# Kernel tuning notes

Measured on AMD Instinct MI355X. Metric: run time of the kernel, lower is better.

## Reference

```python
import jax, jax.numpy as jnp
import numpy as np

K = 3  # knn interpolation neighbors (init kwarg k)
EPS = 1e-8


def _knn_interpolate(x, pos, pos_skip, B, k):
    # Uniform per-batch counts (guaranteed by setup_inputs) let us vectorize the
    # per-batch cdist+topk+gather chain as batched dense ops.
    Nc = pos.shape[0] // B
    Nf = pos_skip.shape[0] // B
    C = x.shape[1]
    pc = pos.reshape(B, Nc, 3)        # coarse positions
    pf = pos_skip.reshape(B, Nf, 3)   # fine (target) positions
    xc = x.reshape(B, Nc, C)          # coarse features
    # squared pairwise distances via gemm: [B, Nf, Nc]
    d2 = (jnp.sum(pf * pf, -1)[:, :, None]
          + jnp.sum(pc * pc, -1)[:, None, :]
          - 2.0 * jnp.einsum('bfd,bcd->bfc', pf, pc))
    _, idx = jax.lax.top_k(-d2, k)    # k nearest coarse indices per fine point
    b = jnp.arange(B)[:, None, None]
    nb_pos = pc[b, idx]                              # [B,Nf,k,3]
    diff = nb_pos - pf[:, :, None, :]
    dist = jnp.sqrt(jnp.sum(diff * diff, -1))        # exact same dist math as torch
    w = 1.0 / (dist + EPS)                           # [B,Nf,k]
    feats = xc[b, idx]                               # [B,Nf,k,C]
    num = jnp.einsum('bfkc,bfk->bfc', feats, w)
    den = jnp.sum(w, -1, keepdims=True) + EPS
    return (num / den).reshape(B * Nf, C)


def setup_inputs() -> dict:
    key = jax.random.key(0)
    ks = jax.random.split(key, 6)
    B, Nc, Nf, C, Cs, H = 16, 1024, 4096, 512, 256, 512
    x = jax.random.normal(ks[0], (B * Nc, C), jnp.float32)
    pos = jax.random.normal(ks[1], (B * Nc, 3), jnp.float32)
    batch = jnp.repeat(jnp.arange(B, dtype=jnp.int64), Nc)
    x_skip = jax.random.normal(ks[2], (B * Nf, Cs), jnp.float32)
    pos_skip = jax.random.normal(ks[3], (B * Nf, 3), jnp.float32)
    batch_skip = jnp.repeat(jnp.arange(B, dtype=jnp.int64), Nf)
    # MLP params (self.nn = MLP 768 -> 512 -> 512, ReLU)
    W1 = jax.random.normal(ks[4], (C + Cs, H), jnp.float32) / np.sqrt(C + Cs).astype(np.float32)
    b1 = jnp.zeros((H,), jnp.float32)
    W2 = jax.random.normal(ks[5], (H, H), jnp.float32) / np.sqrt(H).astype(np.float32)
    b2 = jnp.zeros((H,), jnp.float32)
    return dict(x=x, pos=pos, batch=batch, x_skip=x_skip, pos_skip=pos_skip,
                batch_skip=batch_skip, W1=W1, b1=b1, W2=W2, b2=b2)


def reference(x, pos, batch, x_skip, pos_skip, batch_skip, W1, b1, W2, b2):
    B = int(np.asarray(batch).max()) + 1
    h = _knn_interpolate(x, pos, pos_skip, B, K)   # [N_fine, C]
    h = jnp.concatenate([h, x_skip], axis=1)       # skip connection concat
    h = jax.nn.relu(h @ W1 + b1)
    h = jax.nn.relu(h @ W2 + b2)
    return h
```

## Files before the change

### kernel.cpp

```cpp
#include <hip/hip_runtime.h>
#include <stdint.h>

typedef __attribute__((ext_vector_type(8))) short short8;
typedef __attribute__((ext_vector_type(4))) float f32x4;

static __device__ __forceinline__ ushort f2bf(float f) {
  uint32_t u = __float_as_uint(f);
  uint32_t r = (u + 0x7FFFu + ((u >> 16) & 1u)) >> 16;
  return (ushort)r;
}
static __device__ __forceinline__ float bf2f(ushort h) {
  return __uint_as_float(((uint32_t)h) << 16);
}

static __device__ __forceinline__ void ins3b(double d, int i,
    double& b0, double& b1, double& b2, int& i0, int& i1, int& i2) {
  const bool c0 = d < b0, c1 = d < b1, c2 = d < b2;
  const double nb0 = c0 ? d : b0;
  const int    ni0 = c0 ? i : i0;
  const double nb1 = c0 ? b0 : (c1 ? d : b1);
  const int    ni1 = c0 ? i0 : (c1 ? i : i1);
  const double nb2 = c1 ? b1 : (c2 ? d : b2);
  const int    ni2 = c1 ? i1 : (c2 ? i : i2);
  b0 = nb0; b1 = nb1; b2 = nb2; i0 = ni0; i1 = ni1; i2 = ni2;
}

__global__ __launch_bounds__(256) void prep_kernel(
    const float* __restrict__ pos, const float* __restrict__ pos_skip,
    const float* __restrict__ x, const float* __restrict__ xs,
    const float* __restrict__ W1, const float* __restrict__ W2,
    int4* __restrict__ idx_out, float4* __restrict__ w_out,
    ushort* __restrict__ xbf, ushort* __restrict__ xsbf,
    ushort* __restrict__ W1at, ushort* __restrict__ W1bt,
    ushort* __restrict__ W2t)
{
  __shared__ float pc4[4096];
  if (blockIdx.x < 1024) {
    const int b   = blockIdx.x >> 6;
    const int blk = blockIdx.x & 63;
    for (int i = threadIdx.x; i < 1024; i += 256) {
      const float* ps = pos + (size_t)b * 3072 + i * 3;
      float4 v = { ps[0], ps[1], ps[2], 0.f };
      *(float4*)&pc4[i * 4] = v;
    }
    __syncthreads();

    const int p   = threadIdx.x >> 2;
    const int sub = threadIdx.x & 3;
    const int row = b * 4096 + blk * 64 + p;
    const float pxf = pos_skip[(size_t)row * 3 + 0];
    const float pyf = pos_skip[(size_t)row * 3 + 1];
    const float pzf = pos_skip[(size_t)row * 3 + 2];

    uint32_t c0 = 0xFFFFFFFFu, c1 = 0xFFFFFFFFu, c2 = 0xFFFFFFFFu, c3 = 0xFFFFFFFFu;
    auto ins4u = [&](uint32_t k) {
      const bool l0 = k < c0, l1 = k < c1, l2 = k < c2, l3 = k < c3;
      const uint32_t n0 = l0 ? k  : c0;
      const uint32_t n1 = l0 ? c0 : (l1 ? k : c1);
      const uint32_t n2 = l1 ? c1 : (l2 ? k : c2);
      const uint32_t n3 = l2 ? c2 : (l3 ? k : c3);
      c0 = n0; c1 = n1; c2 = n2; c3 = n3;
    };
#pragma unroll 4
    for (int j = 0; j < 256; ++j) {
      const int i = j * 4 + sub;
      const float4 q = *(const float4*)&pc4[i * 4];
      const float dx = q.x - pxf;
      const float dy = q.y - pyf;
      const float dz = q.z - pzf;
      const float d = fmaf(dx, dx, fmaf(dy, dy, dz * dz));
      ins4u((__float_as_uint(d) & 0xFFFFFC00u) | (uint32_t)i);
    }
#pragma unroll
    for (int m = 1; m <= 2; m <<= 1) {
      const uint32_t e0 = (uint32_t)__shfl_xor((int)c0, m);
      const uint32_t e1 = (uint32_t)__shfl_xor((int)c1, m);
      const uint32_t e2 = (uint32_t)__shfl_xor((int)c2, m);
      const uint32_t e3 = (uint32_t)__shfl_xor((int)c3, m);
      ins4u(e0); ins4u(e1); ins4u(e2); ins4u(e3);
    }
    if (sub == 0) {
      const double pxd = (double)pxf, pyd = (double)pyf, pzd = (double)pzf;
      auto exd = [&](int i) -> double {
        const double dx = (double)pc4[i * 4 + 0] - pxd;
        const double dy = (double)pc4[i * 4 + 1] - pyd;
        const double dz = (double)pc4[i * 4 + 2] - pzd;
        return dx * dx + dy * dy + dz * dz;
      };
      const int j0 = (int)(c0 & 1023u), j1 = (int)(c1 & 1023u);
      const int j2 = (int)(c2 & 1023u), j3 = (int)(c3 & 1023u);
      double b0 = 1e300, b1 = 1e300, b2 = 1e300;
      int i0 = 0, i1 = 0, i2 = 0;
      ins3b(exd(j0), j0, b0, b1, b2, i0, i1, i2);
      ins3b(exd(j1), j1, b0, b1, b2, i0, i1, i2);
      ins3b(exd(j2), j2, b0, b1, b2, i0, i1, i2);
      ins3b(exd(j3), j3, b0, b1, b2, i0, i1, i2);
      const double w0 = 1.0 / (sqrt(b0) + 1e-8);
      const double w1 = 1.0 / (sqrt(b1) + 1e-8);
      const double w2 = 1.0 / (sqrt(b2) + 1e-8);
      const double den = w0 + w1 + w2 + 1e-8;
      idx_out[row] = make_int4(i0, i1, i2, 0);
      w_out[row] = make_float4((float)(w0 / den), (float)(w1 / den), (float)(w2 / den), 0.f);
    }
  } else if (blockIdx.x < 3072) {
    const int id = (blockIdx.x - 1024) * 256 + threadIdx.x;
#pragma unroll
    for (int it = 0; it < 4; ++it) {
      const int i = id + it * 524288;
      const float4 v = *(const float4*)(x + (size_t)i * 4);
      ushort4 o = { f2bf(v.x), f2bf(v.y), f2bf(v.z), f2bf(v.w) };
      *(ushort4*)(xbf + (size_t)i * 4) = o;
    }
  } else if (blockIdx.x < 7168) {
    const int id = (blockIdx.x - 3072) * 256 + threadIdx.x;
#pragma unroll
    for (int it = 0; it < 4; ++it) {
      const int i = id + it * 1048576;
      const float4 v = *(const float4*)(xs + (size_t)i * 4);
      ushort4 o = { f2bf(v.x), f2bf(v.y), f2bf(v.z), f2bf(v.w) };
      *(ushort4*)(xsbf + (size_t)i * 4) = o;
    }
  } else {
    const int id = (blockIdx.x - 7168) * 256 + threadIdx.x;
    if (id < 262144) {
      const int n = id >> 9, k = id & 511;
      W1at[id] = f2bf(W1[(size_t)k * 512 + n]);
    } else if (id < 393216) {
      const int id2 = id - 262144;
      const int n = id2 >> 8, k = id2 & 255;
      W1bt[id2] = f2bf(W1[(size_t)(512 + k) * 512 + n]);
    } else if (id < 655360) {
      const int id3 = id - 393216;
      const int n = id3 >> 9, k = id3 & 511;
      W2t[id3] = f2bf(W2[(size_t)k * 512 + n]);
    }
  }
}

template<int K, bool OUT_BF16, bool ACT, bool COMBINE>
__global__ __launch_bounds__(512, 2) void gemm_bias_relu(
    const ushort* __restrict__ A, const ushort* __restrict__ Bt,
    const float* __restrict__ bias, void* __restrict__ Cout, int M, int N,
    const ushort* __restrict__ Ybf, const int4* __restrict__ idx3,
    const float4* __restrict__ w3)
{
  constexpr int BM = 256, BN = 256, BK = 64, NT = K / BK;
  __shared__ ushort Asm[2][BM * BK];
  __shared__ ushort Bsm[2][BN * BK];
  const int tid  = threadIdx.x;
  const int lane = tid & 63;
  const int wave = tid >> 6;

  const int cpx  = gridDim.x >> 3;
  const int wgid = (blockIdx.x & 7) * cpx + (blockIdx.x >> 3);
  const int nbn  = N / BN;
  const int bm   = wgid / nbn;
  const int bn   = wgid - bm * nbn;
  const int row0 = bm * BM, col0 = bn * BN;
  const int wr = wave >> 2, wc = wave & 3;
  const int sbase = wave * 4096 + lane * 16;

  f32x4 acc[8][4] = {};

  auto stageA = [&](int buf, int kt) {
#pragma unroll
    for (int i = 0; i < 4; ++i) {
      const int o = sbase + i * 1024;
      const int r = o >> 7, s = (o & 127) >> 4;
      __builtin_amdgcn_global_load_lds(
          (const __attribute__((address_space(1))) void*)(A + (size_t)(row0 + r) * K + kt * BK + ((s ^ (r & 7)) << 3)),
          (__attribute__((address_space(3))) void*)((char*)&Asm[buf][0] + o), 16, 0, 0);
    }
  };
  auto stageB = [&](int buf, int kt) {
#pragma unroll
    for (int i = 0; i < 4; ++i) {
      const int o = sbase + i * 1024;
      const int r = o >> 7, s = (o & 127) >> 4;
      __builtin_amdgcn_global_load_lds(
          (const __attribute__((address_space(1))) void*)(Bt + (size_t)(col0 + r) * K + kt * BK + ((s ^ (r & 7)) << 3)),
          (__attribute__((address_space(3))) void*)((char*)&Bsm[buf][0] + o), 16, 0, 0);
    }
  };
  auto rdA = [&](int buf, int mi, int kk) -> short8 {
    const int ra = wr * 128 + mi * 16 + (lane & 15);
    const int s  = kk * 4 + (lane >> 4);
    return *(const short8*)((const char*)&Asm[buf][0] + ra * 128 + ((s ^ (ra & 7)) << 4));
  };
  auto rdB = [&](int buf, int ni, int kk) -> short8 {
    const int rb = wc * 64 + ni * 16 + (lane & 15);
    const int s  = kk * 4 + (lane >> 4);
    return *(const short8*)((const char*)&Bsm[buf][0] + rb * 128 + ((s ^ (rb & 7)) << 4));
  };

  stageA(0, 0); stageB(0, 0);
  asm volatile("s_waitcnt vmcnt(0)" ::: "memory");
  __builtin_amdgcn_s_barrier();

  int cur = 0;
#pragma unroll 1
  for (int t = 0; t < NT; ++t) {
    short8 av[4], bv[4];
#pragma unroll
    for (int mi = 0; mi < 4; ++mi) av[mi] = rdA(cur, mi, 0);
#pragma unroll
    for (int ni = 0; ni < 4; ++ni) bv[ni] = rdB(cur, ni, 0);
    if (t + 1 < NT) stageA(cur ^ 1, t + 1);
    __builtin_amdgcn_s_barrier();
    asm volatile("s_waitcnt lgkmcnt(0)" ::: "memory");
    __builtin_amdgcn_sched_barrier(0);
    __builtin_amdgcn_s_setprio(1);
#pragma unroll
    for (int mi = 0; mi < 4; ++mi)
#pragma unroll
      for (int ni = 0; ni < 4; ++ni)
        acc[mi][ni] = __builtin_amdgcn_mfma_f32_16x16x32_bf16(av[mi], bv[ni], acc[mi][ni], 0, 0, 0);
    __builtin_amdgcn_s_setprio(0);
    __builtin_amdgcn_s_barrier();
#pragma unroll
    for (int mi = 0; mi < 4; ++mi) av[mi] = rdA(cur, 4 + mi, 0);
    if (t + 1 < NT) stageB(cur ^ 1, t + 1);
    __builtin_amdgcn_s_barrier();
    asm volatile("s_waitcnt lgkmcnt(0)" ::: "memory");
    __builtin_amdgcn_sched_barrier(0);
    __builtin_amdgcn_s_setprio(1);
#pragma unroll
    for (int mi = 0; mi < 4; ++mi)
#pragma unroll
      for (int ni = 0; ni < 4; ++ni)
        acc[4 + mi][ni] = __builtin_amdgcn_mfma_f32_16x16x32_bf16(av[mi], bv[ni], acc[4 + mi][ni], 0, 0, 0);
    __builtin_amdgcn_s_setprio(0);
    __builtin_amdgcn_s_barrier();
#pragma unroll
    for (int mi = 0; mi < 4; ++mi) av[mi] = rdA(cur, mi, 1);
#pragma unroll
    for (int ni = 0; ni < 4; ++ni) bv[ni] = rdB(cur, ni, 1);
    __builtin_amdgcn_s_barrier();
    asm volatile("s_waitcnt lgkmcnt(0)" ::: "memory");
    __builtin_amdgcn_sched_barrier(0);
    __builtin_amdgcn_s_setprio(1);
#pragma unroll
    for (int mi = 0; mi < 4; ++mi)
#pragma unroll
      for (int ni = 0; ni < 4; ++ni)
        acc[mi][ni] = __builtin_amdgcn_mfma_f32_16x16x32_bf16(av[mi], bv[ni], acc[mi][ni], 0, 0, 0);
    __builtin_amdgcn_s_setprio(0);
    __builtin_amdgcn_s_barrier();
#pragma unroll
    for (int mi = 0; mi < 4; ++mi) av[mi] = rdA(cur, 4 + mi, 1);
    __builtin_amdgcn_s_barrier();
    asm volatile("s_waitcnt lgkmcnt(0)" ::: "memory");
    __builtin_amdgcn_sched_barrier(0);
    __builtin_amdgcn_s_setprio(1);
#pragma unroll
    for (int mi = 0; mi < 4; ++mi)
#pragma unroll
      for (int ni = 0; ni < 4; ++ni)
        acc[4 + mi][ni] = __builtin_amdgcn_mfma_f32_16x16x32_bf16(av[mi], bv[ni], acc[4 + mi][ni], 0, 0, 0);
    __builtin_amdgcn_s_setprio(0);
    asm volatile("s_waitcnt vmcnt(0)" ::: "memory");
    __builtin_amdgcn_s_barrier();
    cur ^= 1;
  }

  const int lc = lane & 15, lr = lane >> 4;
  if constexpr (COMBINE) {
#pragma unroll
    for (int mi = 0; mi < 8; ++mi) {
#pragma unroll
      for (int r = 0; r < 4; ++r) {
        const int row = row0 + wr * 128 + mi * 16 + lr * 4 + r;
        const int4 id = idx3[row];
        const float4 w = w3[row];
        const ushort* Yb = Ybf + (size_t)(row >> 12) * 524288;
        const ushort* y0 = Yb + (size_t)id.x * 512;
        const ushort* y1 = Yb + (size_t)id.y * 512;
        const ushort* y2 = Yb + (size_t)id.z * 512;
#pragma unroll
        for (int ni = 0; ni < 4; ++ni) {
          const int col = col0 + wc * 64 + ni * 16 + lc;
          float v = acc[mi][ni][r]
                  + w.x * bf2f(y0[col])
                  + w.y * bf2f(y1[col])
                  + w.z * bf2f(y2[col])
                  + bias[col];
          v = v > 0.f ? v : 0.f;
          ((ushort*)Cout)[(size_t)row * 512 + col] = f2bf(v);
        }
      }
    }
  } else {
#pragma unroll
    for (int mi = 0; mi < 8; ++mi) {
#pragma unroll
      for (int ni = 0; ni < 4; ++ni) {
        const int col = col0 + wc * 64 + ni * 16 + lc;
        float bv2 = 0.f;
        if constexpr (ACT) bv2 = bias[col];
        const int rbase = row0 + wr * 128 + mi * 16 + lr * 4;
#pragma unroll
        for (int r = 0; r < 4; ++r) {
          float v = acc[mi][ni][r];
          if constexpr (ACT) { v += bv2; v = v > 0.f ? v : 0.f; }
          if (OUT_BF16) ((ushort*)Cout)[(size_t)(rbase + r) * N + col] = f2bf(v);
          else          ((float*)Cout)[(size_t)(rbase + r) * N + col] = v;
        }
      }
    }
  }
}

extern "C" void kernel_launch(void* const* d_in, const int* in_sizes, int n_in,
                              void* d_out, int out_size, void* d_ws, size_t ws_size,
                              hipStream_t stream) {
  const float* x        = (const float*)d_in[0];
  const float* pos      = (const float*)d_in[1];
  const float* x_skip   = (const float*)d_in[3];
  const float* pos_skip = (const float*)d_in[4];
  const float* W1       = (const float*)d_in[6];
  const float* b1       = (const float*)d_in[7];
  const float* W2       = (const float*)d_in[8];
  const float* b2       = (const float*)d_in[9];

  ushort* Ybf  = (ushort*)d_out;
  ushort* xbf  = (ushort*)((char*)d_out + 83886080);
  ushort* xsbf = (ushort*)((char*)d_out + 100663296);

  char* ws = (char*)d_ws;
  ushort* h2   = (ushort*)ws;
  ushort* W1at = (ushort*)(ws + 67108864);
  ushort* W1bt = (ushort*)(ws + 67633152);
  ushort* W2t  = (ushort*)(ws + 67895296);
  int4*   idx3 = (int4*)  (ws + 68419584);
  float4* w3   = (float4*)(ws + 69468160);

  prep_kernel<<<9728, 256, 0, stream>>>(pos, pos_skip, x, x_skip, W1, W2,
                                        idx3, w3, xbf, xsbf, W1at, W1bt, W2t);
  gemm_bias_relu<512, true, false, false><<<128, 512, 0, stream>>>(
      xbf, W1at, nullptr, (void*)Ybf, 16384, 512, nullptr, nullptr, nullptr);
  gemm_bias_relu<256, true, false, true><<<512, 512, 0, stream>>>(
      xsbf, W1bt, b1, (void*)h2, 65536, 512, Ybf, idx3, w3);
  gemm_bias_relu<512, false, true, false><<<512, 512, 0, stream>>>(
      h2, W2t, b2, d_out, 65536, 512, nullptr, nullptr, nullptr);
}
```

Baseline: 168.8 us.

## Fuse fp32-to-bf16 conversion of x and x_skip into GEMM A-tile staging

```diff
diff --git a/kernel.cpp b/kernel.cpp
--- a/kernel.cpp
+++ b/kernel.cpp
@@ -27,10 +27,8 @@
 
 __global__ __launch_bounds__(256) void prep_kernel(
     const float* __restrict__ pos, const float* __restrict__ pos_skip,
-    const float* __restrict__ x, const float* __restrict__ xs,
     const float* __restrict__ W1, const float* __restrict__ W2,
     int4* __restrict__ idx_out, float4* __restrict__ w_out,
-    ushort* __restrict__ xbf, ushort* __restrict__ xsbf,
     ushort* __restrict__ W1at, ushort* __restrict__ W1bt,
     ushort* __restrict__ W2t)
 {
@@ -102,26 +100,8 @@
       idx_out[row] = make_int4(i0, i1, i2, 0);
       w_out[row] = make_float4((float)(w0 / den), (float)(w1 / den), (float)(w2 / den), 0.f);
     }
-  } else if (blockIdx.x < 3072) {
+  } else {
     const int id = (blockIdx.x - 1024) * 256 + threadIdx.x;
-#pragma unroll
-    for (int it = 0; it < 4; ++it) {
-      const int i = id + it * 524288;
-      const float4 v = *(const float4*)(x + (size_t)i * 4);
-      ushort4 o = { f2bf(v.x), f2bf(v.y), f2bf(v.z), f2bf(v.w) };
-      *(ushort4*)(xbf + (size_t)i * 4) = o;
-    }
-  } else if (blockIdx.x < 7168) {
-    const int id = (blockIdx.x - 3072) * 256 + threadIdx.x;
-#pragma unroll
-    for (int it = 0; it < 4; ++it) {
-      const int i = id + it * 1048576;
-      const float4 v = *(const float4*)(xs + (size_t)i * 4);
-      ushort4 o = { f2bf(v.x), f2bf(v.y), f2bf(v.z), f2bf(v.w) };
-      *(ushort4*)(xsbf + (size_t)i * 4) = o;
-    }
-  } else {
-    const int id = (blockIdx.x - 7168) * 256 + threadIdx.x;
     if (id < 262144) {
       const int n = id >> 9, k = id & 511;
       W1at[id] = f2bf(W1[(size_t)k * 512 + n]);
@@ -137,9 +117,9 @@
   }
 }
 
-template<int K, bool OUT_BF16, bool ACT, bool COMBINE>
+template<int K, bool OUT_BF16, bool ACT, bool COMBINE, bool AF32>
 __global__ __launch_bounds__(512, 2) void gemm_bias_relu(
-    const ushort* __restrict__ A, const ushort* __restrict__ Bt,
+    const void* __restrict__ Av, const ushort* __restrict__ Bt,
     const float* __restrict__ bias, void* __restrict__ Cout, int M, int N,
     const ushort* __restrict__ Ybf, const int4* __restrict__ idx3,
     const float4* __restrict__ w3)
@@ -160,7 +140,12 @@
   const int wr = wave >> 2, wc = wave & 3;
   const int sbase = wave * 4096 + lane * 16;
 
+  const ushort* Abf = (const ushort*)Av;
+  const float*  Af  = (const float*)Av;
+  const int rl = tid >> 1, h = tid & 1;
+
   f32x4 acc[8][4] = {};
+  float4 ga[8];
 
   auto stageA = [&](int buf, int kt) {
 #pragma unroll
@@ -168,8 +153,27 @@
       const int o = sbase + i * 1024;
       const int r = o >> 7, s = (o & 127) >> 4;
       __builtin_amdgcn_global_load_lds(
-          (const __attribute__((address_space(1))) void*)(A + (size_t)(row0 + r) * K + kt * BK + ((s ^ (r & 7)) << 3)),
+          (const __attribute__((address_space(1))) void*)(Abf + (size_t)(row0 + r) * K + kt * BK + ((s ^ (r & 7)) << 3)),
           (__attribute__((address_space(3))) void*)((char*)&Asm[buf][0] + o), 16, 0, 0);
+    }
+  };
+  auto issueA = [&](int kt) {
+    const float* src = Af + (size_t)(row0 + rl) * K + kt * BK + h * 32;
+#pragma unroll
+    for (int q = 0; q < 8; ++q) ga[q] = *(const float4*)(src + q * 4);
+  };
+  auto writeA = [&](int buf) {
+    char* base = (char*)&Asm[buf][0] + rl * 128;
+#pragma unroll
+    for (int q2 = 0; q2 < 4; ++q2) {
+      const int s = h * 4 + q2;
+      short8 o;
+#pragma unroll
+      for (int e = 0; e < 4; ++e) {
+        o[e]     = (short)f2bf(((const float*)&ga[q2 * 2])[e]);
+        o[4 + e] = (short)f2bf(((const float*)&ga[q2 * 2 + 1])[e]);
+      }
+      *(short8*)(base + ((s ^ (rl & 7)) << 4)) = o;
     }
   };
   auto stageB = [&](int buf, int kt) {
@@ -193,8 +197,15 @@
     return *(const short8*)((const char*)&Bsm[buf][0] + rb * 128 + ((s ^ (rb & 7)) << 4));
   };
 
-  stageA(0, 0); stageB(0, 0);
-  asm volatile("s_waitcnt vmcnt(0)" ::: "memory");
+  if constexpr (AF32) {
+    issueA(0); stageB(0, 0);
+    asm volatile("s_waitcnt vmcnt(0)" ::: "memory");
+    writeA(0);
+    asm volatile("s_waitcnt lgkmcnt(0)" ::: "memory");
+  } else {
+    stageA(0, 0); stageB(0, 0);
+    asm volatile("s_waitcnt vmcnt(0)" ::: "memory");
+  }
   __builtin_amdgcn_s_barrier();
 
   int cur = 0;
@@ -205,7 +216,7 @@
     for (int mi = 0; mi < 4; ++mi) av[mi] = rdA(cur, mi, 0);
 #pragma unroll
     for (int ni = 0; ni < 4; ++ni) bv[ni] = rdB(cur, ni, 0);
-    if (t + 1 < NT) stageA(cur ^ 1, t + 1);
+    if (t + 1 < NT) { if constexpr (AF32) issueA(t + 1); else stageA(cur ^ 1, t + 1); }
     __builtin_amdgcn_s_barrier();
     asm volatile("s_waitcnt lgkmcnt(0)" ::: "memory");
     __builtin_amdgcn_sched_barrier(0);
@@ -258,7 +269,15 @@
       for (int ni = 0; ni < 4; ++ni)
         acc[4 + mi][ni] = __builtin_amdgcn_mfma_f32_16x16x32_bf16(av[mi], bv[ni], acc[4 + mi][ni], 0, 0, 0);
     __builtin_amdgcn_s_setprio(0);
-    asm volatile("s_waitcnt vmcnt(0)" ::: "memory");
+    if constexpr (AF32) {
+      if (t + 1 < NT) {
+        asm volatile("s_waitcnt vmcnt(0)" ::: "memory");
+        writeA(cur ^ 1);
+        asm volatile("s_waitcnt lgkmcnt(0)" ::: "memory");
+      }
+    } else {
+      asm volatile("s_waitcnt vmcnt(0)" ::: "memory");
+    }
     __builtin_amdgcn_s_barrier();
     cur ^= 1;
   }
@@ -323,8 +342,6 @@
   const float* b2       = (const float*)d_in[9];
 
   ushort* Ybf  = (ushort*)d_out;
-  ushort* xbf  = (ushort*)((char*)d_out + 83886080);
-  ushort* xsbf = (ushort*)((char*)d_out + 100663296);
 
   char* ws = (char*)d_ws;
   ushort* h2   = (ushort*)ws;
@@ -334,12 +351,12 @@
   int4*   idx3 = (int4*)  (ws + 68419584);
   float4* w3   = (float4*)(ws + 69468160);
 
-  prep_kernel<<<9728, 256, 0, stream>>>(pos, pos_skip, x, x_skip, W1, W2,
-                                        idx3, w3, xbf, xsbf, W1at, W1bt, W2t);
-  gemm_bias_relu<512, true, false, false><<<128, 512, 0, stream>>>(
-      xbf, W1at, nullptr, (void*)Ybf, 16384, 512, nullptr, nullptr, nullptr);
-  gemm_bias_relu<256, true, false, true><<<512, 512, 0, stream>>>(
-      xsbf, W1bt, b1, (void*)h2, 65536, 512, Ybf, idx3, w3);
-  gemm_bias_relu<512, false, true, false><<<512, 512, 0, stream>>>(
+  prep_kernel<<<3584, 256, 0, stream>>>(pos, pos_skip, W1, W2,
+                                        idx3, w3, W1at, W1bt, W2t);
+  gemm_bias_relu<512, true, false, false, true><<<128, 512, 0, stream>>>(
+      x, W1at, nullptr, (void*)Ybf, 16384, 512, nullptr, nullptr, nullptr);
+  gemm_bias_relu<256, true, false, true, true><<<512, 512, 0, stream>>>(
+      x_skip, W1bt, b1, (void*)h2, 65536, 512, Ybf, idx3, w3);
+  gemm_bias_relu<512, false, true, false, false><<<512, 512, 0, stream>>>(
       h2, W2t, b2, d_out, 65536, 512, nullptr, nullptr, nullptr);
 }
```

Measured after the change: 200.7 us. +18.9%, slower.

## Use dedicated 128x128-tile kernel for skip GEMM with fused KNN combine

Applied to the files above, without the earlier changes.

```diff
diff --git a/kernel.cpp b/kernel.cpp
--- a/kernel.cpp
+++ b/kernel.cpp
@@ -137,12 +137,10 @@
   }
 }
 
-template<int K, bool OUT_BF16, bool ACT, bool COMBINE>
+template<int K, bool OUT_BF16, bool ACT>
 __global__ __launch_bounds__(512, 2) void gemm_bias_relu(
     const ushort* __restrict__ A, const ushort* __restrict__ Bt,
-    const float* __restrict__ bias, void* __restrict__ Cout, int M, int N,
-    const ushort* __restrict__ Ybf, const int4* __restrict__ idx3,
-    const float4* __restrict__ w3)
+    const float* __restrict__ bias, void* __restrict__ Cout, int M, int N)
 {
   constexpr int BM = 256, BN = 256, BK = 64, NT = K / BK;
   __shared__ ushort Asm[2][BM * BK];
@@ -264,47 +262,121 @@
   }
 
   const int lc = lane & 15, lr = lane >> 4;
-  if constexpr (COMBINE) {
-#pragma unroll
-    for (int mi = 0; mi < 8; ++mi) {
+#pragma unroll
+  for (int mi = 0; mi < 8; ++mi) {
+#pragma unroll
+    for (int ni = 0; ni < 4; ++ni) {
+      const int col = col0 + wc * 64 + ni * 16 + lc;
+      float bv2 = 0.f;
+      if constexpr (ACT) bv2 = bias[col];
+      const int rbase = row0 + wr * 128 + mi * 16 + lr * 4;
 #pragma unroll
       for (int r = 0; r < 4; ++r) {
-        const int row = row0 + wr * 128 + mi * 16 + lr * 4 + r;
-        const int4 id = idx3[row];
-        const float4 w = w3[row];
-        const ushort* Yb = Ybf + (size_t)(row >> 12) * 524288;
-        const ushort* y0 = Yb + (size_t)id.x * 512;
-        const ushort* y1 = Yb + (size_t)id.y * 512;
-        const ushort* y2 = Yb + (size_t)id.z * 512;
-#pragma unroll
-        for (int ni = 0; ni < 4; ++ni) {
-          const int col = col0 + wc * 64 + ni * 16 + lc;
-          float v = acc[mi][ni][r]
-                  + w.x * bf2f(y0[col])
-                  + w.y * bf2f(y1[col])
-                  + w.z * bf2f(y2[col])
-                  + bias[col];
-          v = v > 0.f ? v : 0.f;
-          ((ushort*)Cout)[(size_t)row * 512 + col] = f2bf(v);
-        }
+        float v = acc[mi][ni][r];
+        if constexpr (ACT) { v += bv2; v = v > 0.f ? v : 0.f; }
+        if (OUT_BF16) ((ushort*)Cout)[(size_t)(rbase + r) * N + col] = f2bf(v);
+        else          ((float*)Cout)[(size_t)(rbase + r) * N + col] = v;
       }
     }
-  } else {
-#pragma unroll
-    for (int mi = 0; mi < 8; ++mi) {
+  }
+}
+
+__global__ __launch_bounds__(256, 2) void gemm128_combine(
+    const ushort* __restrict__ A, const ushort* __restrict__ Bt,
+    const float* __restrict__ bias, ushort* __restrict__ h2,
+    const ushort* __restrict__ Ybf, const int4* __restrict__ idx3,
+    const float4* __restrict__ w3)
+{
+  constexpr int K = 256, N = 512, BM = 128, BN = 128, BK = 64, NT = K / BK;
+  __shared__ ushort Asm[2][BM * BK];
+  __shared__ ushort Bsm[2][BN * BK];
+  const int tid  = threadIdx.x;
+  const int lane = tid & 63;
+  const int wave = tid >> 6;
+
+  const int cpx  = gridDim.x >> 3;
+  const int wgid = (blockIdx.x & 7) * cpx + (blockIdx.x >> 3);
+  const int nbn  = N / BN;
+  const int bm   = wgid / nbn;
+  const int bn   = wgid - bm * nbn;
+  const int row0 = bm * BM, col0 = bn * BN;
+  const int wr = wave >> 1, wc = wave & 1;
+  const int so = tid * 16;
+
+  f32x4 acc[4][4] = {};
+
+  auto stage = [&](int buf, int kt) {
+#pragma unroll
+    for (int i = 0; i < 4; ++i) {
+      const int o = i * 4096 + so;
+      const int r = o >> 7, s = (o & 127) >> 4;
+      const int cu = ((s ^ (r & 7)) << 3);
+      __builtin_amdgcn_global_load_lds(
+          (const __attribute__((address_space(1))) void*)(A + (size_t)(row0 + r) * K + kt * BK + cu),
+          (__attribute__((address_space(3))) void*)((char*)&Asm[buf][0] + o), 16, 0, 0);
+      __builtin_amdgcn_global_load_lds(
+          (const __attribute__((address_space(1))) void*)(Bt + (size_t)(col0 + r) * K + kt * BK + cu),
+          (__attribute__((address_space(3))) void*)((char*)&Bsm[buf][0] + o), 16, 0, 0);
+    }
+  };
+  auto compute = [&](int buf) {
+#pragma unroll
+    for (int kk = 0; kk < 2; ++kk) {
+      short8 af[4], bfr[4];
+#pragma unroll
+      for (int mi = 0; mi < 4; ++mi) {
+        const int ra = wr * 64 + mi * 16 + (lane & 15);
+        const int s  = kk * 4 + (lane >> 4);
+        af[mi] = *(const short8*)&Asm[buf][ra * BK + ((s ^ (ra & 7)) << 3)];
+      }
+#pragma unroll
+      for (int ni = 0; ni < 4; ++ni) {
+        const int rb = wc * 64 + ni * 16 + (lane & 15);
+        const int s  = kk * 4 + (lane >> 4);
+        bfr[ni] = *(const short8*)&Bsm[buf][rb * BK + ((s ^ (rb & 7)) << 3)];
+      }
+#pragma unroll
+      for (int mi = 0; mi < 4; ++mi)
+#pragma unroll
+        for (int ni = 0; ni < 4; ++ni)
+          acc[mi][ni] = __builtin_amdgcn_mfma_f32_16x16x32_bf16(af[mi], bfr[ni], acc[mi][ni], 0, 0, 0);
+    }
+  };
+
+  stage(0, 0);
+  __syncthreads();
+  int cur = 0;
+#pragma unroll 1
+  for (int kt = 0; kt < NT - 1; ++kt) {
+    stage(cur ^ 1, kt + 1);
+    compute(cur);
+    __syncthreads();
+    cur ^= 1;
+  }
+  compute(cur);
+
+  const int lc = lane & 15, lr = lane >> 4;
+#pragma unroll
+  for (int mi = 0; mi < 4; ++mi) {
+#pragma unroll
+    for (int r = 0; r < 4; ++r) {
+      const int row = row0 + wr * 64 + mi * 16 + lr * 4 + r;
+      const int4 id = idx3[row];
+      const float4 w = w3[row];
+      const ushort* Yb = Ybf + (size_t)(row >> 12) * 524288;
+      const ushort* y0 = Yb + (size_t)id.x * 512;
+      const ushort* y1 = Yb + (size_t)id.y * 512;
+      const ushort* y2 = Yb + (size_t)id.z * 512;
 #pragma unroll
       for (int ni = 0; ni < 4; ++ni) {
         const int col = col0 + wc * 64 + ni * 16 + lc;
-        float bv2 = 0.f;
-        if constexpr (ACT) bv2 = bias[col];
-        const int rbase = row0 + wr * 128 + mi * 16 + lr * 4;
-#pragma unroll
-        for (int r = 0; r < 4; ++r) {
-          float v = acc[mi][ni][r];
-          if constexpr (ACT) { v += bv2; v = v > 0.f ? v : 0.f; }
-          if (OUT_BF16) ((ushort*)Cout)[(size_t)(rbase + r) * N + col] = f2bf(v);
-          else          ((float*)Cout)[(size_t)(rbase + r) * N + col] = v;
-        }
+        float v = acc[mi][ni][r]
+                + w.x * bf2f(y0[col])
+                + w.y * bf2f(y1[col])
+                + w.z * bf2f(y2[col])
+                + bias[col];
+        v = v > 0.f ? v : 0.f;
+        h2[(size_t)row * 512 + col] = f2bf(v);
       }
     }
   }
@@ -336,10 +408,9 @@
 
   prep_kernel<<<9728, 256, 0, stream>>>(pos, pos_skip, x, x_skip, W1, W2,
                                         idx3, w3, xbf, xsbf, W1at, W1bt, W2t);
-  gemm_bias_relu<512, true, false, false><<<128, 512, 0, stream>>>(
-      xbf, W1at, nullptr, (void*)Ybf, 16384, 512, nullptr, nullptr, nullptr);
-  gemm_bias_relu<256, true, false, true><<<512, 512, 0, stream>>>(
-      xsbf, W1bt, b1, (void*)h2, 65536, 512, Ybf, idx3, w3);
-  gemm_bias_relu<512, false, true, false><<<512, 512, 0, stream>>>(
-      h2, W2t, b2, d_out, 65536, 512, nullptr, nullptr, nullptr);
-}
+  gemm_bias_relu<512, true, false><<<128, 512, 0, stream>>>(
+      xbf, W1at, nullptr, (void*)Ybf, 16384, 512);
+  gemm128_combine<<<2048, 256, 0, stream>>>(xsbf, W1bt, b1, h2, Ybf, idx3, w3);
+  gemm_bias_relu<512, false, true><<<512, 512, 0, stream>>>(
+      h2, W2t, b2, d_out, 65536, 512);
+}
```

Result: no change. 170.0 us (+0.7%).
